# Optimization experiments

Measured on AMD Instinct MI355X. Metric: run time of the kernel, lower is better.

The kernel has to match this reference:

```python
import jax, jax.numpy as jnp
import numpy as np

CAP = 15.0
EPS = 1e-6
NUM_HEADS = 16
HEAD_DIM = 64

def _rmsnorm(x, w):
    xf = x.astype(jnp.float32)
    var = jnp.mean(xf * xf, axis=-1, keepdims=True)
    return w * (xf * jax.lax.rsqrt(var + EPS)).astype(x.dtype)

def _gate(g):
    # sigmoid(soft_cap(g)) with cap 15
    return jax.nn.sigmoid(CAP * jnp.tanh(g / CAP))

def setup_inputs() -> dict:
    key = jax.random.key(0)
    ks = jax.random.split(key, 4)
    B, S, D = 4, 2048, 1024
    H, Dh = NUM_HEADS, HEAD_DIM
    return {
        "x": jax.random.normal(ks[0], (B, S, D), jnp.float32),
        "hidden_state": jnp.zeros((B, H, Dh, Dh), jnp.float32),
        "w_rms": jnp.ones((D,), jnp.float32),
        "w_qkv": jax.random.normal(ks[1], (D, 3 * H * Dh), jnp.float32) * 0.02,
        "w_gate": jax.random.normal(ks[2], (D, 3 * H), jnp.float32) * 0.02,
        "w_out": jax.random.normal(ks[3], (D, D), jnp.float32) * 0.02,
    }

def reference(x, hidden_state, w_rms, w_qkv, w_gate, w_out):
    B, S, D = x.shape
    H, Dh = NUM_HEADS, HEAD_DIM
    residual = x
    xn = _rmsnorm(x, w_rms)
    qkv = (xn @ w_qkv).reshape(B, S, 3, H, Dh)
    q, k, v = qkv[:, :, 0], qkv[:, :, 1], qkv[:, :, 2]  # [B,S,H,Dh]
    gates = _gate((xn @ w_gate).reshape(B, S, 3, H))
    i_g, f_g, o_g = gates[:, :, 0], gates[:, :, 1], gates[:, :, 2]  # [B,S,H]

    # time-major for scan: [S,B,H,...]
    def tm(a):
        return jnp.moveaxis(a, 1, 0)

    def step(state, inp):
        qt, kt, vt, it, ft, ot = inp  # [B,H,Dh]/[B,H]
        kv = kt[..., :, None] * vt[..., None, :]            # [B,H,Dh,Dh]
        state = ft[..., None, None] * state + it[..., None, None] * kv
        h = jnp.einsum('bhd,bhde->bhe', qt, state) * ot[..., None]
        return state, h

    _, h_seq = jax.lax.scan(step, hidden_state,
                            (tm(q), tm(k), tm(v), tm(i_g), tm(f_g), tm(o_g)))
    out = jnp.moveaxis(h_seq, 0, 1).reshape(B, S, H * Dh) @ w_out
    return residual + out
```

## Files before the change

kernel.cpp:

```cpp
#include <hip/hip_runtime.h>
#include <math.h>

typedef unsigned short u16;
typedef unsigned int   u32;
typedef __bf16 bf16x8 __attribute__((ext_vector_type(8)));
typedef float  f32x4  __attribute__((ext_vector_type(4)));

#define NBATCH 4
#define SEQ    2048
#define DIM    1024
#define NH     16
#define BH     64
#define NC     32
#define ROWS   8192
#define N1     3328

__device__ __forceinline__ u16 f2bf(float f) {
  u32 u = __builtin_bit_cast(u32, f);
  u32 r = u + 0x7fffu + ((u >> 16) & 1u);
  return (u16)(r >> 16);
}
__device__ __forceinline__ float bf2f(u16 h) {
  return __builtin_bit_cast(float, (u32)h << 16);
}

__device__ __forceinline__ void gl2lds16(const u16* g, u16* l) {
  __builtin_amdgcn_global_load_lds(
      (const __attribute__((address_space(1))) u32*)g,
      (__attribute__((address_space(3))) u32*)l, 16, 0, 0);
}

__global__ __launch_bounds__(256) void transpose_w(const float* __restrict__ W,
                                                   u16* __restrict__ Bt, int K, int N) {
  __shared__ float tile[32][33];
  const int n0 = blockIdx.x * 32, k0 = blockIdx.y * 32;
  const int tx = threadIdx.x, ty = threadIdx.y;
  #pragma unroll
  for (int i = 0; i < 4; i++)
    tile[ty + i * 8][tx] = W[(size_t)(k0 + ty + i * 8) * N + n0 + tx];
  __syncthreads();
  #pragma unroll
  for (int i = 0; i < 4; i++)
    Bt[(size_t)(n0 + ty + i * 8) * K + k0 + tx] = f2bf(tile[tx][ty + i * 8]);
}

__global__ __launch_bounds__(256) void fill_gateW(const float* __restrict__ wg,
                                                  u16* __restrict__ Bt) {
  const int g = blockIdx.x;
  const int tid = threadIdx.x;
  #pragma unroll
  for (int kk = 0; kk < 4; kk++) {
    const int k = kk * 256 + tid;
    u16 v = 0;
    if (g < 48) v = f2bf(wg[(size_t)k * 48 + g]);
    Bt[(size_t)(3072 + g) * 1024 + k] = v;
  }
}

__global__ __launch_bounds__(256) void rmsnorm_k(const float* __restrict__ x,
                                                 const float* __restrict__ w,
                                                 u16* __restrict__ xn) {
  const int row = blockIdx.x, tid = threadIdx.x;
  const float4 xv = *(const float4*)&x[(size_t)row * 1024 + tid * 4];
  float ss = xv.x * xv.x + xv.y * xv.y + xv.z * xv.z + xv.w * xv.w;
  #pragma unroll
  for (int off = 32; off > 0; off >>= 1) ss += __shfl_down(ss, off);
  __shared__ float red[4];
  if ((tid & 63) == 0) red[tid >> 6] = ss;
  __syncthreads();
  const float tot = red[0] + red[1] + red[2] + red[3];
  const float scale = rsqrtf(tot * (1.0f / 1024.0f) + 1e-6f);
  const float4 wv = *(const float4*)&w[tid * 4];
  const u16 o0 = f2bf(xv.x * scale * wv.x), o1 = f2bf(xv.y * scale * wv.y);
  const u16 o2 = f2bf(xv.z * scale * wv.z), o3 = f2bf(xv.w * scale * wv.w);
  uint2 ov;
  ov.x = (u32)o0 | ((u32)o1 << 16);
  ov.y = (u32)o2 | ((u32)o3 << 16);
  *(uint2*)&xn[(size_t)row * 1024 + tid * 4] = ov;
}


#define FENCE asm volatile("" ::: "memory")
#define SBAR  do { FENCE; __builtin_amdgcn_s_barrier(); FENCE; } while (0)
#define WAITV4 do { FENCE; asm volatile("s_waitcnt vmcnt(4)" ::: "memory"); } while (0)
#define WAITV0 do { FENCE; asm volatile("s_waitcnt vmcnt(0)" ::: "memory"); } while (0)

#define STAGE_A(BUF, HALF, TILE) do { \
  const u16* s_ = Abase + (size_t)(TILE) * 64 + (size_t)(HALF) * 131072; \
  u16* l_ = &lds[((BUF) * 4 + (HALF)) * 8192 + tid * 8]; \
  gl2lds16(s_, l_); gl2lds16(s_ + 65536, l_ + 4096); \
} while (0)

#define STAGE_B(BUF, HALF, TILE) do { \
  const u16* s_ = Bbase + (size_t)(TILE) * 64 + (size_t)(HALF) * 131072; \
  u16* l_ = &lds[((BUF) * 4 + 2 + (HALF)) * 8192 + tid * 8]; \
  gl2lds16(s_, l_); gl2lds16(s_ + 65536, l_ + 4096); \
} while (0)

#define READ_A(ALDS, MH) do { \
  _Pragma("unroll") \
  for (int mi_ = 0; mi_ < 4; ++mi_) { \
    af[mi_][0] = *(const bf16x8*)((ALDS) + (MH) * 4096 + mi_ * 1024 + co0); \
    af[mi_][1] = *(const bf16x8*)((ALDS) + (MH) * 4096 + mi_ * 1024 + co1); \
  } \
} while (0)

#define READ_B(BLDS, NH) do { \
  _Pragma("unroll") \
  for (int ni_ = 0; ni_ < 2; ++ni_) { \
    bfr[NH][ni_][0] = *(const bf16x8*)((BLDS) + (NH) * 2048 + ni_ * 1024 + co0); \
    bfr[NH][ni_][1] = *(const bf16x8*)((BLDS) + (NH) * 2048 + ni_ * 1024 + co1); \
  } \
} while (0)

#define MFMA16(MH, NH) do { \
  __builtin_amdgcn_s_setprio(1); \
  _Pragma("unroll") \
  for (int mi_ = 0; mi_ < 4; ++mi_) { \
    _Pragma("unroll") \
    for (int ni_ = 0; ni_ < 2; ++ni_) { \
      acc[(MH)*4+mi_][(NH)*2+ni_] = __builtin_amdgcn_mfma_f32_16x16x32_bf16( \
          af[mi_][0], bfr[NH][ni_][0], acc[(MH)*4+mi_][(NH)*2+ni_], 0, 0, 0); \
      acc[(MH)*4+mi_][(NH)*2+ni_] = __builtin_amdgcn_mfma_f32_16x16x32_bf16( \
          af[mi_][1], bfr[NH][ni_][1], acc[(MH)*4+mi_][(NH)*2+ni_], 0, 0, 0); \
    } \
  } \
  __builtin_amdgcn_s_setprio(0); \
} while (0)

#define GITER(T, FULL) do { \
   READ_A(aLds0, 0); READ_B(bLds0, 0); STAGE_A(1, 0, 2*(T)+1); \
         SBAR; MFMA16(0, 0); SBAR; \
   READ_B(bLds0, 1); STAGE_A(1, 1, 2*(T)+1); \
         SBAR; MFMA16(0, 1); SBAR; \
   READ_A(aLds0, 1); if (FULL) STAGE_B(0, 0, 2*(T)+2); \
         SBAR; MFMA16(1, 0); SBAR; \
   if (FULL) STAGE_B(0, 1, 2*(T)+2); \
         SBAR; MFMA16(1, 1); if (FULL) { WAITV4; } else { WAITV0; } SBAR; \
   READ_A(aLds1, 0); READ_B(bLds1, 0); if (FULL) STAGE_A(0, 0, 2*(T)+2); \
         SBAR; MFMA16(0, 0); SBAR; \
   READ_B(bLds1, 1); if (FULL) STAGE_A(0, 1, 2*(T)+2); \
         SBAR; MFMA16(0, 1); SBAR; \
   READ_A(aLds1, 1); if (FULL) STAGE_B(1, 0, 2*(T)+3); \
         SBAR; MFMA16(1, 0); SBAR; \
   if (FULL) STAGE_B(1, 1, 2*(T)+3); \
         SBAR; MFMA16(1, 1); if (FULL) { WAITV4; } SBAR; \
} while (0)

#define CORE_SETUP(AROWBASE, BCOLBASE) \
  const int tid = threadIdx.x; \
  const int lane = tid & 63, wave = tid >> 6; \
  const int q = lane >> 4, m16 = lane & 15; \
  const int wm = wave & 1, wn = wave >> 1; \
  const int sx = m16 & 7; \
  const int co0 = (q ^ sx) * 8; \
  const int co1 = ((4 + q) ^ sx) * 8; \
  const int r0 = tid >> 3, pc = tid & 7; \
  const int lcg = pc ^ (r0 & 7); \
  const u16* Abase = (AROWBASE) + (size_t)r0 * 1024 + lcg * 8; \
  const u16* Bbase = (BCOLBASE) + (size_t)r0 * 1024 + lcg * 8; \
  const u16* aLds0 = &lds[wm * 8192 + m16 * 64]; \
  const u16* aLds1 = aLds0 + 32768; \
  const u16* bLds0 = &lds[16384 + (wn >> 1) * 8192 + ((wn & 1) * 64 + m16) * 64]; \
  const u16* bLds1 = bLds0 + 32768; \
  bf16x8 af[4][2]; \
  bf16x8 bfr[2][2][2]; \
  f32x4 acc[8][4] = {};

#define CORE_RUN16() do { \
  STAGE_A(0, 0, 0); STAGE_A(0, 1, 0); STAGE_B(0, 0, 0); STAGE_B(0, 1, 0); \
  STAGE_B(1, 0, 1); STAGE_B(1, 1, 1); \
  WAITV4; SBAR; \
  _Pragma("unroll 1") \
  for (int t = 0; t < 7; ++t) GITER(t, 1); \
  GITER(7, 0); \
} while (0)

__global__ __launch_bounds__(512, 2) void gemm_qkv(const u16* __restrict__ A, const u16* __restrict__ Bt,
                                                   u16* __restrict__ Qb, u16* __restrict__ Kb,
                                                   u16* __restrict__ Vb, float* __restrict__ gates) {
  __shared__ __attribute__((aligned(16))) u16 lds[65536];

  const int g = blockIdx.x;
  const int swz = (g & 7) * 52 + (g >> 3);
  const int bm = swz & 31, bn = swz >> 5;
  const int rowBase = bm * 256, colBase = bn * 256;

  CORE_SETUP(A + (size_t)rowBase * 1024, Bt + (size_t)colBase * 1024);
  CORE_RUN16();

  const int rr = lane >> 2, co = (lane & 3) * 16;
  if (colBase < 3072) {
    const int which = colBase >> 10;
    u16* dstBase = (which == 0) ? Qb : ((which == 1) ? Kb : Vb);
    const int b = rowBase >> 11;
    const int h = ((colBase & 1023) >> 6) + wn;
    const int tRow0 = (rowBase & 2047) + wm * 128;
    u16* headBase = dstBase + ((size_t)(b * 16 + h)) * 2048 * 64;
    u16* scratch = lds + wave * 1024;
    #pragma unroll
    for (int mi = 0; mi < 8; ++mi) {
      #pragma unroll
      for (int bj = 0; bj < 4; ++bj)
        #pragma unroll
        for (int r = 0; r < 4; ++r)
          scratch[(q * 4 + r) * 64 + bj * 16 + m16] = f2bf(acc[mi][bj][r]);
      const uint4 d0 = *(const uint4*)&scratch[rr * 64 + co];
      const uint4 d1 = *(const uint4*)&scratch[rr * 64 + co + 8];
      u16* gp = headBase + (size_t)(tRow0 + mi * 16 + rr) * 64 + co;
      *(uint4*)gp = d0;
      *(uint4*)(gp + 8) = d1;
    }
  } else {
    if (wn == 0) {
      #pragma unroll
      for (int ai = 0; ai < 8; ++ai)
        #pragma unroll
        for (int bj = 0; bj < 3; ++bj)
          #pragma unroll
          for (int r = 0; r < 4; ++r) {
            const int grow = rowBase + wm * 128 + ai * 16 + q * 4 + r;
            const int b = grow >> 11, tt = grow & 2047;
            const float v = acc[ai][bj][r];
            const float gg = 1.0f / (1.0f + __expf(-(15.0f * tanhf(v * (1.0f / 15.0f)))));
            gates[((size_t)bj * 64 + (b * 16 + m16)) * 2048 + tt] = gg;
          }
    }
  }
}

__global__ __launch_bounds__(512, 2) void gemm_out(const u16* __restrict__ A, const u16* __restrict__ Bt,
                                                   const float* __restrict__ resid,
                                                   float* __restrict__ out) {
  __shared__ __attribute__((aligned(16))) u16 lds[65536];

  const int g = blockIdx.x;
  const int swz = (g & 7) * 16 + (g >> 3);
  const int bm = swz & 31, bn = swz >> 5;
  const int rowBase = bm * 256, colBase = bn * 256;

  CORE_SETUP(A + (size_t)rowBase * 1024, Bt + (size_t)colBase * 1024);
  CORE_RUN16();

  const int colW = colBase + (wn >> 1) * 128 + (wn & 1) * 64;
  #pragma unroll
  for (int mi = 0; mi < 8; ++mi)
    #pragma unroll
    for (int bj = 0; bj < 4; ++bj)
      #pragma unroll
      for (int r = 0; r < 4; ++r) {
        const int grow = rowBase + wm * 128 + mi * 16 + q * 4 + r;
        const int gcol = colW + bj * 16 + m16;
        const size_t idx = (size_t)grow * 1024 + gcol;
        out[idx] = acc[mi][bj][r] + resid[idx];
      }
}

__global__ __launch_bounds__(256) void passA_k(const u16* __restrict__ Qb, const u16* __restrict__ Kb,
                                               const u16* __restrict__ Vb,
                                               const float* __restrict__ gates,
                                               float* __restrict__ la,
                                               u16* __restrict__ Mbuf, u16* __restrict__ hseq) {
  __shared__ u16 Ql[64][72], Kl[64][72], KTl[64][72], VTl[64][72], Pl[64][72];
  __shared__ float laS[64], iS[64];
  const int tid = threadIdx.x;
  const int bh = blockIdx.x >> 5, c = blockIdx.x & 31;
  const int lane = tid & 63, w = tid >> 6;
  const int q = lane >> 4, m16 = lane & 15;
  const size_t base = ((size_t)bh * 2048 + c * 64) * 64;
  const int toff = c * 64;

  if (tid < 64) {
    float lg = __logf(gates[(size_t)(64 + bh) * 2048 + toff + tid]);
    #pragma unroll
    for (int off = 1; off < 64; off <<= 1) {
      const float y = __shfl_up(lg, off);
      if (tid >= off) lg += y;
    }
    laS[tid] = lg;
    iS[tid] = gates[(size_t)bh * 2048 + toff + tid];
    la[(size_t)bh * 2048 + toff + tid] = lg;
  }
  __syncthreads();

  {
    const int s = tid >> 2, db = (tid & 3) * 16;
    const float wk = __expf(laS[63] - laS[s]) * iS[s];
    const uint4 q0 = *(const uint4*)&Qb[base + s * 64 + db];
    const uint4 q1 = *(const uint4*)&Qb[base + s * 64 + db + 8];
    *(uint4*)&Ql[s][db] = q0;
    *(uint4*)&Ql[s][db + 8] = q1;
    const uint4 k0 = *(const uint4*)&Kb[base + s * 64 + db];
    const uint4 k1 = *(const uint4*)&Kb[base + s * 64 + db + 8];
    *(uint4*)&Kl[s][db] = k0;
    *(uint4*)&Kl[s][db + 8] = k1;
    u16 ktmp[16];
    *(uint4*)&ktmp[0] = k0;
    *(uint4*)&ktmp[8] = k1;
    #pragma unroll
    for (int j = 0; j < 16; j++) KTl[db + j][s] = f2bf(wk * bf2f(ktmp[j]));
    const uint4 v0 = *(const uint4*)&Vb[base + s * 64 + db];
    const uint4 v1 = *(const uint4*)&Vb[base + s * 64 + db + 8];
    u16 vtmp[16];
    *(uint4*)&vtmp[0] = v0;
    *(uint4*)&vtmp[8] = v1;
    #pragma unroll
    for (int j = 0; j < 16; j++) VTl[db + j][s] = vtmp[j];
  }
  __syncthreads();

  f32x4 pacc[4] = {};
  #pragma unroll
  for (int ks = 0; ks < 2; ks++) {
    const bf16x8 aq = *(const bf16x8*)&Ql[w * 16 + m16][ks * 32 + q * 8];
    #pragma unroll
    for (int ni = 0; ni < 4; ni++) {
      const bf16x8 bk = *(const bf16x8*)&Kl[ni * 16 + m16][ks * 32 + q * 8];
      pacc[ni] = __builtin_amdgcn_mfma_f32_16x16x32_bf16(aq, bk, pacc[ni], 0, 0, 0);
    }
  }
  #pragma unroll
  for (int ni = 0; ni < 4; ni++)
    #pragma unroll
    for (int r = 0; r < 4; r++) {
      const int tt = w * 16 + q * 4 + r, ss = ni * 16 + m16;
      float Wts = 0.0f;
      if (ss <= tt) Wts = __expf(laS[tt] - laS[ss]) * iS[ss];
      Pl[tt][ss] = f2bf(pacc[ni][r] * Wts);
    }
  __syncthreads();

  f32x4 hacc[4] = {}, macc[4] = {};
  #pragma unroll
  for (int ks = 0; ks < 2; ks++) {
    const bf16x8 ap = *(const bf16x8*)&Pl[w * 16 + m16][ks * 32 + q * 8];
    const bf16x8 av = *(const bf16x8*)&VTl[w * 16 + m16][ks * 32 + q * 8];
    #pragma unroll
    for (int ni = 0; ni < 4; ni++) {
      const bf16x8 bv = *(const bf16x8*)&VTl[ni * 16 + m16][ks * 32 + q * 8];
      const bf16x8 bk = *(const bf16x8*)&KTl[ni * 16 + m16][ks * 32 + q * 8];
      hacc[ni] = __builtin_amdgcn_mfma_f32_16x16x32_bf16(ap, bv, hacc[ni], 0, 0, 0);
      macc[ni] = __builtin_amdgcn_mfma_f32_16x16x32_bf16(av, bk, macc[ni], 0, 0, 0);
    }
  }

  __syncthreads();
  #pragma unroll
  for (int ni = 0; ni < 4; ni++)
    #pragma unroll
    for (int r = 0; r < 4; r++) {
      const int tt = w * 16 + q * 4 + r, e = ni * 16 + m16;
      Pl[tt][e] = f2bf(hacc[ni][r]);
      Kl[tt][e] = f2bf(macc[ni][r]);
    }
  __syncthreads();
  {
    const int s = tid >> 2, db = (tid & 3) * 16;
    const int b = bh >> 4, h = bh & 15;
    u16* hp = &hseq[((size_t)b * 2048 + c * 64 + s) * 1024 + h * 64 + db];
    *(uint4*)hp       = *(const uint4*)&Pl[s][db];
    *(uint4*)(hp + 8) = *(const uint4*)&Pl[s][db + 8];
    u16* mp = &Mbuf[(((size_t)bh * 32 + c) * 64 + s) * 64 + db];
    *(uint4*)mp       = *(const uint4*)&Kl[s][db];
    *(uint4*)(mp + 8) = *(const uint4*)&Kl[s][db + 8];
  }
}

__global__ __launch_bounds__(256) void passB_k(u16* __restrict__ Mbuf,
                                               const float* __restrict__ hidden,
                                               const float* __restrict__ la) {
  const int bh = blockIdx.x >> 4;
  const int e = (blockIdx.x & 15) * 256 + threadIdx.x;
  __shared__ float Gs[32];
  if (threadIdx.x < 32)
    Gs[threadIdx.x] = __expf(la[(size_t)bh * 2048 + threadIdx.x * 64 + 63]);
  __syncthreads();
  const int eRow = e >> 6, dCol = e & 63;
  float st = hidden[(size_t)bh * 4096 + dCol * 64 + eRow];
  u16* M = &Mbuf[(size_t)bh * 32 * 4096 + e];
  float m_next = bf2f(M[0]);
  #pragma unroll 4
  for (int c = 0; c < 32; c++) {
    const float m_cur = m_next;
    if (c < 31) m_next = bf2f(M[(size_t)(c + 1) * 4096]);
    M[(size_t)c * 4096] = f2bf(st);
    st = Gs[c] * st + m_cur;
  }
}

__global__ __launch_bounds__(256) void passC_k(const u16* __restrict__ Qb,
                                               const u16* __restrict__ SprevT,
                                               const float* __restrict__ la,
                                               const float* __restrict__ gates,
                                               u16* __restrict__ hseq) {
  __shared__ u16 aQl[64][72], STl[64][72];
  __shared__ float hstage[64][68];
  __shared__ float laS[64], oS[64];
  const int tid = threadIdx.x;
  const int bh = blockIdx.x >> 5, c = blockIdx.x & 31;
  const int lane = tid & 63, w = tid >> 6;
  const int q = lane >> 4, m16 = lane & 15;
  const size_t base = ((size_t)bh * 2048 + c * 64) * 64;
  const int toff = c * 64;
  if (tid < 64) {
    laS[tid] = la[(size_t)bh * 2048 + toff + tid];
    oS[tid] = gates[(size_t)(128 + bh) * 2048 + toff + tid];
  }
  {
    const int s = tid >> 2, db = (tid & 3) * 16;
    *(uint4*)&aQl[s][db]     = *(const uint4*)&Qb[base + s * 64 + db];
    *(uint4*)&aQl[s][db + 8] = *(const uint4*)&Qb[base + s * 64 + db + 8];
    const u16* SpT = &SprevT[((size_t)bh * 32 + c) * 4096];
    *(uint4*)&STl[s][db]     = *(const uint4*)&SpT[s * 64 + db];
    *(uint4*)&STl[s][db + 8] = *(const uint4*)&SpT[s * 64 + db + 8];
  }
  __syncthreads();
  f32x4 acc[4] = {};
  #pragma unroll
  for (int ks = 0; ks < 2; ks++) {
    const bf16x8 a = *(const bf16x8*)&aQl[w * 16 + m16][ks * 32 + q * 8];
    #pragma unroll
    for (int ni = 0; ni < 4; ni++) {
      const bf16x8 bb = *(const bf16x8*)&STl[ni * 16 + m16][ks * 32 + q * 8];
      acc[ni] = __builtin_amdgcn_mfma_f32_16x16x32_bf16(a, bb, acc[ni], 0, 0, 0);
    }
  }
  #pragma unroll
  for (int ni = 0; ni < 4; ni++)
    #pragma unroll
    for (int r = 0; r < 4; r++)
      hstage[w * 16 + q * 4 + r][ni * 16 + m16] = acc[ni][r];
  __syncthreads();
  {
    const int s = tid >> 2, db = (tid & 3) * 16;
    const int b = bh >> 4, h = bh & 15;
    const float a_t = __expf(laS[s]);
    const float o = oS[s];
    u16* hp = &hseq[((size_t)b * 2048 + c * 64 + s) * 1024 + h * 64 + db];
    uint4 h0 = *(const uint4*)hp, h1 = *(const uint4*)(hp + 8);
    u16 hv[16];
    *(uint4*)&hv[0] = h0;
    *(uint4*)&hv[8] = h1;
    float sv[16];
    *(float4*)&sv[0]  = *(const float4*)&hstage[s][db];
    *(float4*)&sv[4]  = *(const float4*)&hstage[s][db + 4];
    *(float4*)&sv[8]  = *(const float4*)&hstage[s][db + 8];
    *(float4*)&sv[12] = *(const float4*)&hstage[s][db + 12];
    u16 ov[16];
    #pragma unroll
    for (int j = 0; j < 16; j++)
      ov[j] = f2bf(o * (bf2f(hv[j]) + a_t * sv[j]));
    *(uint4*)hp       = *(const uint4*)&ov[0];
    *(uint4*)(hp + 8) = *(const uint4*)&ov[8];
  }
}

extern "C" void kernel_launch(void* const* d_in, const int* in_sizes, int n_in,
                              void* d_out, int out_size, void* d_ws, size_t ws_size,
                              hipStream_t stream) {
  (void)in_sizes; (void)n_in; (void)out_size; (void)ws_size;
  const float* x      = (const float*)d_in[0];
  const float* hidden = (const float*)d_in[1];
  const float* w_rms  = (const float*)d_in[2];
  const float* w_qkv  = (const float*)d_in[3];
  const float* w_gate = (const float*)d_in[4];
  const float* w_out  = (const float*)d_in[5];
  float* out = (float*)d_out;

  char* p = (char*)d_ws;
  u16* wqkvT = (u16*)p;  p += (size_t)N1 * 1024 * 2;
  u16* woutT = (u16*)p;  p += (size_t)1024 * 1024 * 2;
  u16* xn    = (u16*)p;  p += (size_t)ROWS * 1024 * 2;
  u16* Qb    = (u16*)p;  p += (size_t)BH * 2048 * 64 * 2;
  u16* Kb    = (u16*)p;  p += (size_t)BH * 2048 * 64 * 2;
  u16* Vb    = (u16*)p;  p += (size_t)BH * 2048 * 64 * 2;
  float* gates = (float*)p; p += (size_t)3 * BH * 2048 * 4;
  float* la    = (float*)p; p += (size_t)BH * 2048 * 4;
  u16* Mbuf  = (u16*)p;  p += (size_t)BH * NC * 4096 * 2;
  u16* hseq  = (u16*)p;  p += (size_t)ROWS * 1024 * 2;

  transpose_w<<<dim3(96, 32), dim3(32, 8), 0, stream>>>(w_qkv, wqkvT, 1024, 3072);
  transpose_w<<<dim3(32, 32), dim3(32, 8), 0, stream>>>(w_out, woutT, 1024, 1024);
  fill_gateW<<<256, 256, 0, stream>>>(w_gate, wqkvT);
  rmsnorm_k<<<ROWS, 256, 0, stream>>>(x, w_rms, xn);
  gemm_qkv<<<416, 512, 0, stream>>>(xn, wqkvT, Qb, Kb, Vb, gates);
  passA_k<<<BH * NC, 256, 0, stream>>>(Qb, Kb, Vb, gates, la, Mbuf, hseq);
  passB_k<<<BH * 16, 256, 0, stream>>>(Mbuf, hidden, la);
  passC_k<<<BH * NC, 256, 0, stream>>>(Qb, Mbuf, la, gates, hseq);
  gemm_out<<<128, 512, 0, stream>>>(hseq, woutT, x, out);
}
```

Before: 259.6 us.

## Merge weight-prep kernels into one launch and coarsen GEMM barrier phases

Combines the two weight transposes and the gate-weight fill into a single prep_w launch, so two kernel launches and their gaps go away. The gate fill now runs as 32 extra blocks, each covering 8 gate rows (48 real rows plus zero padding up to 256). Separately, the GEMM main loop is restructured from eight barrier-separated MFMA phases per iteration to four, issuing two MFMA16 groups between barriers and batching the LDS reads and global stages. This cuts barrier count but holds more fragments live and gives less fine-grained interleaving of loads and MFMAs.

```diff
diff --git a/kernel.cpp b/kernel.cpp
--- a/kernel.cpp
+++ b/kernel.cpp
@@ -30,30 +30,39 @@
       (__attribute__((address_space(3))) u32*)l, 16, 0, 0);
 }
 
-__global__ __launch_bounds__(256) void transpose_w(const float* __restrict__ W,
-                                                   u16* __restrict__ Bt, int K, int N) {
-  __shared__ float tile[32][33];
-  const int n0 = blockIdx.x * 32, k0 = blockIdx.y * 32;
+__global__ __launch_bounds__(256) void prep_w(const float* __restrict__ Wqkv,
+                                              const float* __restrict__ Wout,
+                                              const float* __restrict__ wg,
+                                              u16* __restrict__ BtQkv, u16* __restrict__ BtOut) {
+  const int bx = blockIdx.x;
   const int tx = threadIdx.x, ty = threadIdx.y;
-  #pragma unroll
-  for (int i = 0; i < 4; i++)
-    tile[ty + i * 8][tx] = W[(size_t)(k0 + ty + i * 8) * N + n0 + tx];
-  __syncthreads();
-  #pragma unroll
-  for (int i = 0; i < 4; i++)
-    Bt[(size_t)(n0 + ty + i * 8) * K + k0 + tx] = f2bf(tile[tx][ty + i * 8]);
-}
-
-__global__ __launch_bounds__(256) void fill_gateW(const float* __restrict__ wg,
-                                                  u16* __restrict__ Bt) {
-  const int g = blockIdx.x;
-  const int tid = threadIdx.x;
-  #pragma unroll
-  for (int kk = 0; kk < 4; kk++) {
-    const int k = kk * 256 + tid;
-    u16 v = 0;
-    if (g < 48) v = f2bf(wg[(size_t)k * 48 + g]);
-    Bt[(size_t)(3072 + g) * 1024 + k] = v;
+  if (bx < 128) {
+    const float* W; u16* Bt; int N, n0;
+    if (bx < 96) { W = Wqkv; Bt = BtQkv; N = 3072; n0 = bx * 32; }
+    else         { W = Wout; Bt = BtOut; N = 1024; n0 = (bx - 96) * 32; }
+    const int k0 = blockIdx.y * 32;
+    __shared__ float tile[32][33];
+    #pragma unroll
+    for (int i = 0; i < 4; i++)
+      tile[ty + i * 8][tx] = W[(size_t)(k0 + ty + i * 8) * N + n0 + tx];
+    __syncthreads();
+    #pragma unroll
+    for (int i = 0; i < 4; i++)
+      Bt[(size_t)(n0 + ty + i * 8) * 1024 + k0 + tx] = f2bf(tile[tx][ty + i * 8]);
+  } else {
+    const int tid = ty * 32 + tx;
+    const int gy = blockIdx.y;
+    #pragma unroll
+    for (int gg = 0; gg < 8; gg++) {
+      const int g = gy * 8 + gg;
+      #pragma unroll
+      for (int kk = 0; kk < 4; kk++) {
+        const int k = kk * 256 + tid;
+        u16 v = 0;
+        if (g < 48) v = f2bf(wg[(size_t)k * 48 + g]);
+        BtQkv[(size_t)(3072 + g) * 1024 + k] = v;
+      }
+    }
   }
 }
 
@@ -128,23 +137,23 @@
   __builtin_amdgcn_s_setprio(0); \
 } while (0)
 
-#define GITER(T, FULL) do { \
-   READ_A(aLds0, 0); READ_B(bLds0, 0); STAGE_A(1, 0, 2*(T)+1); \
-         SBAR; MFMA16(0, 0); SBAR; \
-   READ_B(bLds0, 1); STAGE_A(1, 1, 2*(T)+1); \
-         SBAR; MFMA16(0, 1); SBAR; \
-   READ_A(aLds0, 1); if (FULL) STAGE_B(0, 0, 2*(T)+2); \
-         SBAR; MFMA16(1, 0); SBAR; \
-   if (FULL) STAGE_B(0, 1, 2*(T)+2); \
-         SBAR; MFMA16(1, 1); if (FULL) { WAITV4; } else { WAITV0; } SBAR; \
-   READ_A(aLds1, 0); READ_B(bLds1, 0); if (FULL) STAGE_A(0, 0, 2*(T)+2); \
-         SBAR; MFMA16(0, 0); SBAR; \
-   READ_B(bLds1, 1); if (FULL) STAGE_A(0, 1, 2*(T)+2); \
-         SBAR; MFMA16(0, 1); SBAR; \
-   READ_A(aLds1, 1); if (FULL) STAGE_B(1, 0, 2*(T)+3); \
-         SBAR; MFMA16(1, 0); SBAR; \
-   if (FULL) STAGE_B(1, 1, 2*(T)+3); \
-         SBAR; MFMA16(1, 1); if (FULL) { WAITV4; } SBAR; \
+#define GITER4(T, FULL) do { \
+   \
+  READ_A(aLds0, 0); READ_B(bLds0, 0); READ_B(bLds0, 1); \
+  STAGE_A(1, 0, 2*(T)+1); STAGE_A(1, 1, 2*(T)+1); \
+  SBAR; MFMA16(0, 0); MFMA16(0, 1); SBAR; \
+   \
+  READ_A(aLds0, 1); \
+  if (FULL) { STAGE_B(0, 0, 2*(T)+2); STAGE_B(0, 1, 2*(T)+2); } \
+  SBAR; MFMA16(1, 0); MFMA16(1, 1); if (FULL) { WAITV4; } else { WAITV0; } SBAR; \
+   \
+  READ_A(aLds1, 0); READ_B(bLds1, 0); READ_B(bLds1, 1); \
+  if (FULL) { STAGE_A(0, 0, 2*(T)+2); STAGE_A(0, 1, 2*(T)+2); } \
+  SBAR; MFMA16(0, 0); MFMA16(0, 1); SBAR; \
+   \
+  READ_A(aLds1, 1); \
+  if (FULL) { STAGE_B(1, 0, 2*(T)+3); STAGE_B(1, 1, 2*(T)+3); } \
+  SBAR; MFMA16(1, 0); MFMA16(1, 1); if (FULL) { WAITV4; } SBAR; \
 } while (0)
 
 #define CORE_SETUP(AROWBASE, BCOLBASE) \
@@ -172,8 +181,8 @@
   STAGE_B(1, 0, 1); STAGE_B(1, 1, 1); \
   WAITV4; SBAR; \
   _Pragma("unroll 1") \
-  for (int t = 0; t < 7; ++t) GITER(t, 1); \
-  GITER(7, 0); \
+  for (int t = 0; t < 7; ++t) GITER4(t, 1); \
+  GITER4(7, 0); \
 } while (0)
 
 __global__ __launch_bounds__(512, 2) void gemm_qkv(const u16* __restrict__ A, const u16* __restrict__ Bt,
@@ -479,9 +488,7 @@
   u16* Mbuf  = (u16*)p;  p += (size_t)BH * NC * 4096 * 2;
   u16* hseq  = (u16*)p;  p += (size_t)ROWS * 1024 * 2;
 
-  transpose_w<<<dim3(96, 32), dim3(32, 8), 0, stream>>>(w_qkv, wqkvT, 1024, 3072);
-  transpose_w<<<dim3(32, 32), dim3(32, 8), 0, stream>>>(w_out, woutT, 1024, 1024);
-  fill_gateW<<<256, 256, 0, stream>>>(w_gate, wqkvT);
+  prep_w<<<dim3(129, 32), dim3(32, 8), 0, stream>>>(w_qkv, w_out, w_gate, wqkvT, woutT);
   rmsnorm_k<<<ROWS, 256, 0, stream>>>(x, w_rms, xn);
   gemm_qkv<<<416, 512, 0, stream>>>(xn, wqkvT, Qb, Kb, Vb, gates);
   passA_k<<<BH * NC, 256, 0, stream>>>(Qb, Kb, Vb, gates, la, Mbuf, hseq);
```

Result: no change. 255.8 us (-1.5%).
